# Optimization experiments

Measured on AMD Instinct MI355X. Metric: run time of the kernel, lower is better.

Reference implementation:

```python
import jax, jax.numpy as jnp
import numpy as np

H = 128  # GRU hidden dim

def gru_sequence(x_emb, W_ih, W_hh, b_ih, b_hh):
    """Run a GRU over x_emb (S, B, E); return final-step output (B, H).
    Matches torch.nn.GRU gate math:
      r = sig(W_ir x + b_ir + W_hr h + b_hr)
      z = sig(W_iz x + b_iz + W_hz h + b_hz)
      n = tanh(W_in x + b_in + r * (W_hn h + b_hn))
      h' = (1 - z) * n + z * h
    """
    S, B, E = x_emb.shape
    # Precompute input projections for all timesteps: (S, B, 3H)
    gx_all = jnp.einsum('sbe,ge->sbg', x_emb, W_ih) + b_ih

    def step(h, gx):
        gh = h @ W_hh.T + b_hh               # (B, 3H)
        r = jax.nn.sigmoid(gx[:, :H] + gh[:, :H])
        z = jax.nn.sigmoid(gx[:, H:2*H] + gh[:, H:2*H])
        n = jnp.tanh(gx[:, 2*H:] + r * gh[:, 2*H:])
        h_new = (1.0 - z) * n + z * h
        return h_new, None

    h0 = jnp.zeros((B, H), dtype=x_emb.dtype)
    h_final, _ = jax.lax.scan(step, h0, gx_all)
    return h_final  # (B, H) == out at last timestep


def setup_inputs() -> dict:
    key = jax.random.key(0)
    ks = jax.random.split(key, 12)
    S, B, V, E = 512, 512, 50000, 50
    x1 = jax.random.randint(ks[0], (S, B), 0, V, dtype=jnp.int32)
    x2 = jax.random.randint(ks[1], (S, B), 0, V, dtype=jnp.int32)
    emb = jax.random.uniform(ks[2], (V, E), jnp.float32, -0.01, 0.01)
    s = 1.0 / np.sqrt(H)
    W_ih = jax.random.uniform(ks[3], (3*H, E), jnp.float32, -s, s)
    W_hh = jax.random.uniform(ks[4], (3*H, H), jnp.float32, -s, s)
    b_ih = jax.random.uniform(ks[5], (3*H,), jnp.float32, -s, s)
    b_hh = jax.random.uniform(ks[6], (3*H,), jnp.float32, -s, s)
    s1 = 1.0 / np.sqrt(2*H)
    W1 = jax.random.uniform(ks[7], (H, 2*H), jnp.float32, -s1, s1)
    b1 = jax.random.uniform(ks[8], (H,), jnp.float32, -s1, s1)
    s2 = 1.0 / np.sqrt(H)
    W2 = jax.random.uniform(ks[9], (1, H), jnp.float32, -s2, s2)
    b2 = jax.random.uniform(ks[10], (1,), jnp.float32, -s2, s2)
    return {"x1": x1, "x2": x2, "emb": emb, "W_ih": W_ih, "W_hh": W_hh,
            "b_ih": b_ih, "b_hh": b_hh, "W1": W1, "b1": b1, "W2": W2, "b2": b2}


def reference(x1, x2, emb, W_ih, W_hh, b_ih, b_hh, W1, b1, W2, b2):
    e1 = emb[x1]  # (S, B, E)
    e2 = emb[x2]
    h1 = gru_sequence(e1, W_ih, W_hh, b_ih, b_hh)  # (B, H)
    h2 = gru_sequence(e2, W_ih, W_hh, b_ih, b_hh)  # (B, H)
    fc_in = jnp.concatenate([h1, h2], axis=-1)     # (B, 2H)
    hid = jax.nn.relu(fc_in @ W1.T + b1)
    out = jax.nn.sigmoid(hid @ W2.T + b2)          # (B, 1)
    return out
```

## Files before the change

### kernel.cpp

```cpp
#include <hip/hip_runtime.h>
#include <hip/hip_bf16.h>
#include <stdint.h>

#define S_LEN 512
#define BATCH 512
#define HID   128
#define G3    384
#define EMB   50
#define VOC   50000

#define NL2E  (-1.4426950408889634f)
#define N2L2E (-2.8853900817779268f)

typedef __attribute__((ext_vector_type(8))) short short8;
typedef __attribute__((ext_vector_type(4))) float float4v;

__device__ inline unsigned short f2bf(float f) {
  union { float f; uint32_t u; } v; v.f = f;
  uint32_t u = v.u;
  u += 0x7fffu + ((u >> 16) & 1u);
  return (unsigned short)(u >> 16);
}
__device__ inline float bf2f(unsigned short h) {
  union { uint32_t u; float f; } v; v.u = ((uint32_t)h) << 16;
  return v.f;
}
__device__ inline uint32_t fbits(float f) {
  union { float f; uint32_t u; } v; v.f = f; return v.u;
}
__device__ inline float fast_sig(float x) {
  return __builtin_amdgcn_rcpf(1.f + __expf(-x));
}

__global__ __launch_bounds__(128) void prep_wih(
    const float* __restrict__ W_ih, const float* __restrict__ b_ih,
    const float* __restrict__ b_hh, unsigned short* __restrict__ wbf,
    float* __restrict__ sbias) {
  const int nt = blockIdx.x;
  const int kf = threadIdx.x >> 6;
  const int L  = threadIdx.x & 63;
  const int q = L >> 4, ln = L & 15;
  const int g = nt * 16 + ln;
  const float sc = (g < 256) ? NL2E : N2L2E;
  const int k0 = kf * 32 + q * 8;
  short8 v;
#pragma unroll
  for (int i = 0; i < 8; ++i) {
    const int k = k0 + i;
    v[i] = (k < EMB) ? (short)f2bf(W_ih[(size_t)g * EMB + k] * sc) : (short)0;
  }
  *(short8*)(wbf + (size_t)((nt * 2 + kf) * 64 + L) * 8) = v;
  if (threadIdx.x < 16) {
    const int gg = nt * 16 + threadIdx.x;
    const float s2 = (gg < 256) ? NL2E : N2L2E;
    sbias[gg] = s2 * (b_ih[gg] + (gg < 256 ? b_hh[gg] : 0.f));
  }
}

__global__ __launch_bounds__(256) void build_gxv(
    const float* __restrict__ emb, const unsigned short* __restrict__ wbf,
    const float* __restrict__ sbias, unsigned short* __restrict__ gxv) {
  __shared__ __align__(16) unsigned short cmat[64][392];
  const int w  = threadIdx.x >> 6;
  const int L  = threadIdx.x & 63;
  const int q  = L >> 4;
  const int ln = L & 15;
  const int vbase = blockIdx.x * 64 + w * 16;
  const int vloc  = w * 16;

  const int vr = min(vbase + ln, VOC - 1);
  const float* arow = emb + (size_t)vr * EMB;
  float fa[16];
#pragma unroll
  for (int i = 0; i < 16; ++i) {
    const int k = ((i < 8) ? q * 8 : 32 + q * 8 - 8) + i;
    fa[i] = 0.f;
  }
  short8 afr0, afr1;
  {
    float f[8];
#pragma unroll
    for (int i = 0; i < 8; ++i) { const int k = q * 8 + i; f[i] = (k < EMB) ? arow[k] : 0.f; }
#pragma unroll
    for (int i = 0; i < 8; ++i) afr0[i] = (short)f2bf(f[i]);
#pragma unroll
    for (int i = 0; i < 8; ++i) { const int k = 32 + q * 8 + i; f[i] = (k < EMB) ? arow[k] : 0.f; }
#pragma unroll
    for (int i = 0; i < 8; ++i) afr1[i] = (short)f2bf(f[i]);
  }

  for (int nt = 0; nt < 24; ++nt) {
    const short8 b0 = *(const short8*)(wbf + (size_t)((nt * 2 + 0) * 64 + L) * 8);
    const short8 b1 = *(const short8*)(wbf + (size_t)((nt * 2 + 1) * 64 + L) * 8);
    const int gg = nt * 16 + ln;
    const float bias = sbias[gg];
    float4v acc = {bias, bias, bias, bias};
    acc = __builtin_amdgcn_mfma_f32_16x16x32_bf16(afr0, b0, acc, 0, 0, 0);
    acc = __builtin_amdgcn_mfma_f32_16x16x32_bf16(afr1, b1, acc, 0, 0, 0);
#pragma unroll
    for (int r = 0; r < 4; ++r)
      cmat[vloc + q * 4 + r][gg] = f2bf(acc[r]);
  }
  __syncthreads();

  for (int idx = threadIdx.x; idx < 3072; idx += 256) {
    const int row = idx / 48, c8 = idx - row * 48;
    const int vrow = blockIdx.x * 64 + row;
    if (vrow < VOC) {
      short8 v = *(const short8*)(&cmat[row][c8 * 8]);
      *(short8*)(gxv + (size_t)vrow * G3 + c8 * 8) = v;
    }
  }
}

__global__ __launch_bounds__(512) void gru_kernel(
    const int* __restrict__ x1, const int* __restrict__ x2,
    const unsigned short* __restrict__ gxv, const float* __restrict__ W_hh,
    const float* __restrict__ b_hh, float* __restrict__ fcin) {
  const int bid   = blockIdx.x;
  const int gru   = bid >> 7;
  const int chunk = bid & 127;
  const int* xs   = gru ? x2 : x1;

  const int tid = threadIdx.x;
  const int w  = tid >> 6;
  const int L  = tid & 63;
  const int q  = L >> 4;
  const int ln = L & 15;
  const int jb = w * 16;
  const int g3 = ln >> 2;
  const int n  = ln & 3;
  const int j  = jb + q * 4 + g3;
  const int ng = chunk * 4 + n;

  __shared__ __align__(16) unsigned short hbuf[2][512];

  short8 afrag[3][4];
#pragma unroll
  for (int t = 0; t < 3; ++t) {
    const float sc = (t < 2) ? NL2E : N2L2E;
    const float* wr = W_hh + (size_t)(t * 128 + jb + ln) * HID;
#pragma unroll
    for (int kf = 0; kf < 4; ++kf) {
      const int k0 = kf * 32 + q * 8;
      float4v f0 = *(const float4v*)(wr + k0);
      float4v f1 = *(const float4v*)(wr + k0 + 4);
      short8 a;
#pragma unroll
      for (int i = 0; i < 4; ++i) a[i] = (short)f2bf(f0[i] * sc);
#pragma unroll
      for (int i = 0; i < 4; ++i) a[i + 4] = (short)f2bf(f1[i] * sc);
      afrag[t][kf] = a;
    }
  }

  float4v bhn4;
#pragma unroll
  for (int r = 0; r < 4; ++r) bhn4[r] = N2L2E * b_hh[2 * 128 + jb + q * 4 + r];

  for (int idx = tid; idx < 1024; idx += 512) ((unsigned short*)hbuf)[idx] = 0;

  float h = 0.f;

  unsigned short gxr, gxz, gxnn, nr, nz, nn2;
  {
    const unsigned short* gp = gxv + (size_t)xs[ng] * G3;
    gxr = gp[j]; gxz = gp[128 + j]; gxnn = gp[256 + j];
    const unsigned short* gq = gxv + (size_t)xs[BATCH + ng] * G3;
    nr = gq[j]; nz = gq[128 + j]; nn2 = gq[256 + j];
  }
  int tokf = xs[2 * BATCH + ng];

  const int wofs = (((j >> 3) * 4 + n) << 3) + (j & 7);
  const int rofs = ((q * 4 + n) << 3);

  const bool selA = (ln & 4) != 0;
  const bool selB = (ln & 8) != 0;

  __syncthreads();

  for (int s = 0; s < S_LEN; ++s) {
    unsigned short fr, fz, fn;
    {
      const unsigned short* gp = gxv + (size_t)tokf * G3;
      fr = gp[j]; fz = gp[128 + j]; fn = gp[256 + j];
    }
    const int s3 = (s + 3 < S_LEN) ? (s + 3) : 0;
    const int tok3 = xs[s3 * BATCH + ng];

    const unsigned short* rb = hbuf[s & 1];
    short8 bfrag[4];
#pragma unroll
    for (int kf = 0; kf < 4; ++kf)
      bfrag[kf] = *(const short8*)(rb + kf * 128 + rofs);

    float vsel[3];
#pragma unroll
    for (int t = 0; t < 3; ++t) {
      float4v a0 = (t == 2) ? bhn4 : (float4v){0.f, 0.f, 0.f, 0.f};
      float4v a1 = {0.f, 0.f, 0.f, 0.f};
      a0 = __builtin_amdgcn_mfma_f32_16x16x32_bf16(afrag[t][0], bfrag[0], a0, 0, 0, 0);
      a1 = __builtin_amdgcn_mfma_f32_16x16x32_bf16(afrag[t][1], bfrag[1], a1, 0, 0, 0);
      a0 = __builtin_amdgcn_mfma_f32_16x16x32_bf16(afrag[t][2], bfrag[2], a0, 0, 0, 0);
      a1 = __builtin_amdgcn_mfma_f32_16x16x32_bf16(afrag[t][3], bfrag[3], a1, 0, 0, 0);
      const float4v acc = a0 + a1;
      const float x0 = selA ? acc[1] : acc[0];
      const float x1 = selA ? acc[3] : acc[2];
      vsel[t] = selB ? x1 : x0;
    }

    const float gr = bf2f(gxr) + vsel[0];
    const float gz = bf2f(gxz) + vsel[1];
    const float rg = __builtin_amdgcn_rcpf(1.f + __builtin_amdgcn_exp2f(gr));
    const float zg = __builtin_amdgcn_rcpf(1.f + __builtin_amdgcn_exp2f(gz));
    const float pre = bf2f(gxnn) + rg * vsel[2];
    const float sg  = __builtin_amdgcn_rcpf(1.f + __builtin_amdgcn_exp2f(pre));
    const float nn  = 2.f * sg - 1.f;
    h = zg * (h - nn) + nn;

    hbuf[(s + 1) & 1][wofs] = (unsigned short)((fbits(h) + 0x8000u) >> 16);

    asm volatile("s_waitcnt lgkmcnt(0)\n\ts_barrier" ::: "memory");

    gxr = nr; gxz = nz; gxnn = nn2;
    nr = fr; nz = fz; nn2 = fn;
    tokf = tok3;
  }

  fcin[(size_t)ng * 256 + gru * 128 + j] = h;
}

__global__ __launch_bounds__(128) void head_kernel(
    const float* __restrict__ fcin, const float* __restrict__ W1,
    const float* __restrict__ b1, const float* __restrict__ W2,
    const float* __restrict__ b2, float* __restrict__ out) {
  __shared__ float fc[256];
  __shared__ float part[2];
  const int b = blockIdx.x, t = threadIdx.x;
  fc[t]       = fcin[(size_t)b * 256 + t];
  fc[t + 128] = fcin[(size_t)b * 256 + t + 128];
  __syncthreads();

  float acc = b1[t];
#pragma unroll 8
  for (int k = 0; k < 256; ++k) acc += W1[t * 256 + k] * fc[k];
  const float hid = fmaxf(acc, 0.f);

  float v = hid * W2[t];
#pragma unroll
  for (int o = 32; o > 0; o >>= 1) v += __shfl_xor(v, o, 64);
  if ((t & 63) == 0) part[t >> 6] = v;
  __syncthreads();
  if (t == 0) {
    const float s = part[0] + part[1] + b2[0];
    out[b] = fast_sig(s);
  }
}

extern "C" void kernel_launch(void* const* d_in, const int* in_sizes, int n_in,
                              void* d_out, int out_size, void* d_ws, size_t ws_size,
                              hipStream_t stream) {
  const int*   x1   = (const int*)d_in[0];
  const int*   x2   = (const int*)d_in[1];
  const float* emb  = (const float*)d_in[2];
  const float* W_ih = (const float*)d_in[3];
  const float* W_hh = (const float*)d_in[4];
  const float* b_ih = (const float*)d_in[5];
  const float* b_hh = (const float*)d_in[6];
  const float* W1   = (const float*)d_in[7];
  const float* b1   = (const float*)d_in[8];
  const float* W2   = (const float*)d_in[9];
  const float* b2   = (const float*)d_in[10];
  float* out = (float*)d_out;

  char* ws = (char*)d_ws;
  unsigned short* gxv = (unsigned short*)ws;
  float* fcin = (float*)(ws + (size_t)VOC * G3 * 2);
  unsigned short* wbf = (unsigned short*)(ws + (size_t)VOC * G3 * 2 + 524288);
  float* sbias = (float*)(ws + (size_t)VOC * G3 * 2 + 524288 + 49152);

  prep_wih<<<24, 128, 0, stream>>>(W_ih, b_ih, b_hh, wbf, sbias);
  build_gxv<<<(VOC + 63) / 64, 256, 0, stream>>>(emb, wbf, sbias, gxv);
  gru_kernel<<<256, 512, 0, stream>>>(x1, x2, gxv, W_hh, b_hh, fcin);
  head_kernel<<<512, 128, 0, stream>>>(fcin, W1, b1, W2, b2, out);
}
```

Measured before the change: 346.7 us.

## Interleave r/z gate projections into packed 32-bit table to cut per-step gathers

```diff
diff --git a/kernel.cpp b/kernel.cpp
--- a/kernel.cpp
+++ b/kernel.cpp
@@ -21,9 +21,8 @@
   u += 0x7fffu + ((u >> 16) & 1u);
   return (unsigned short)(u >> 16);
 }
-__device__ inline float bf2f(unsigned short h) {
-  union { uint32_t u; float f; } v; v.u = ((uint32_t)h) << 16;
-  return v.f;
+__device__ inline float bitsf(uint32_t u) {
+  union { uint32_t u; float f; } v; v.u = u; return v.f;
 }
 __device__ inline uint32_t fbits(float f) {
   union { float f; uint32_t u; } v; v.f = f; return v.u;
@@ -59,8 +58,10 @@
 
 __global__ __launch_bounds__(256) void build_gxv(
     const float* __restrict__ emb, const unsigned short* __restrict__ wbf,
-    const float* __restrict__ sbias, unsigned short* __restrict__ gxv) {
-  __shared__ __align__(16) unsigned short cmat[64][392];
+    const float* __restrict__ sbias, uint32_t* __restrict__ gxrz,
+    unsigned short* __restrict__ gxn) {
+  __shared__ __align__(16) unsigned short crz[64][264];
+  __shared__ __align__(16) unsigned short cn[64][136];
   const int w  = threadIdx.x >> 6;
   const int L  = threadIdx.x & 63;
   const int q  = L >> 4;
@@ -70,25 +71,22 @@
 
   const int vr = min(vbase + ln, VOC - 1);
   const float* arow = emb + (size_t)vr * EMB;
-  float fa[16];
-#pragma unroll
-  for (int i = 0; i < 16; ++i) {
-    const int k = ((i < 8) ? q * 8 : 32 + q * 8 - 8) + i;
-    fa[i] = 0.f;
-  }
   short8 afr0, afr1;
   {
-    float f[8];
-#pragma unroll
-    for (int i = 0; i < 8; ++i) { const int k = q * 8 + i; f[i] = (k < EMB) ? arow[k] : 0.f; }
-#pragma unroll
-    for (int i = 0; i < 8; ++i) afr0[i] = (short)f2bf(f[i]);
-#pragma unroll
-    for (int i = 0; i < 8; ++i) { const int k = 32 + q * 8 + i; f[i] = (k < EMB) ? arow[k] : 0.f; }
-#pragma unroll
-    for (int i = 0; i < 8; ++i) afr1[i] = (short)f2bf(f[i]);
-  }
-
+    float f;
+#pragma unroll
+    for (int i = 0; i < 8; ++i) {
+      const int k = q * 8 + i; f = (k < EMB) ? arow[k] : 0.f;
+      afr0[i] = (short)f2bf(f);
+    }
+#pragma unroll
+    for (int i = 0; i < 8; ++i) {
+      const int k = 32 + q * 8 + i; f = (k < EMB) ? arow[k] : 0.f;
+      afr1[i] = (short)f2bf(f);
+    }
+  }
+
+#pragma unroll 2
   for (int nt = 0; nt < 24; ++nt) {
     const short8 b0 = *(const short8*)(wbf + (size_t)((nt * 2 + 0) * 64 + L) * 8);
     const short8 b1 = *(const short8*)(wbf + (size_t)((nt * 2 + 1) * 64 + L) * 8);
@@ -97,26 +95,45 @@
     float4v acc = {bias, bias, bias, bias};
     acc = __builtin_amdgcn_mfma_f32_16x16x32_bf16(afr0, b0, acc, 0, 0, 0);
     acc = __builtin_amdgcn_mfma_f32_16x16x32_bf16(afr1, b1, acc, 0, 0, 0);
-#pragma unroll
-    for (int r = 0; r < 4; ++r)
-      cmat[vloc + q * 4 + r][gg] = f2bf(acc[r]);
+    if (nt < 8) {
+      const int j = gg;
+#pragma unroll
+      for (int r = 0; r < 4; ++r) crz[vloc + q * 4 + r][2 * j] = f2bf(acc[r]);
+    } else if (nt < 16) {
+      const int j = gg - 128;
+#pragma unroll
+      for (int r = 0; r < 4; ++r) crz[vloc + q * 4 + r][2 * j + 1] = f2bf(acc[r]);
+    } else {
+      const int j = gg - 256;
+#pragma unroll
+      for (int r = 0; r < 4; ++r) cn[vloc + q * 4 + r][j] = f2bf(acc[r]);
+    }
   }
   __syncthreads();
 
-  for (int idx = threadIdx.x; idx < 3072; idx += 256) {
-    const int row = idx / 48, c8 = idx - row * 48;
+  for (int idx = threadIdx.x; idx < 2048; idx += 256) {
+    const int row = idx >> 5, c8 = idx & 31;
     const int vrow = blockIdx.x * 64 + row;
     if (vrow < VOC) {
-      short8 v = *(const short8*)(&cmat[row][c8 * 8]);
-      *(short8*)(gxv + (size_t)vrow * G3 + c8 * 8) = v;
+      short8 v = *(const short8*)(&crz[row][c8 * 8]);
+      *(short8*)((unsigned short*)gxrz + (size_t)vrow * 256 + c8 * 8) = v;
+    }
+  }
+  for (int idx = threadIdx.x; idx < 1024; idx += 256) {
+    const int row = idx >> 4, c8 = idx & 15;
+    const int vrow = blockIdx.x * 64 + row;
+    if (vrow < VOC) {
+      short8 v = *(const short8*)(&cn[row][c8 * 8]);
+      *(short8*)(gxn + (size_t)vrow * 128 + c8 * 8) = v;
     }
   }
 }
 
 __global__ __launch_bounds__(512) void gru_kernel(
     const int* __restrict__ x1, const int* __restrict__ x2,
-    const unsigned short* __restrict__ gxv, const float* __restrict__ W_hh,
-    const float* __restrict__ b_hh, float* __restrict__ fcin) {
+    const uint32_t* __restrict__ gxrz, const unsigned short* __restrict__ gxn,
+    const float* __restrict__ W_hh, const float* __restrict__ b_hh,
+    float* __restrict__ fcin) {
   const int bid   = blockIdx.x;
   const int gru   = bid >> 7;
   const int chunk = bid & 127;
@@ -162,12 +179,13 @@
 
   float h = 0.f;
 
-  unsigned short gxr, gxz, gxnn, nr, nz, nn2;
+  uint32_t rzc, rz1;
+  unsigned short nc, n1;
   {
-    const unsigned short* gp = gxv + (size_t)xs[ng] * G3;
-    gxr = gp[j]; gxz = gp[128 + j]; gxnn = gp[256 + j];
-    const unsigned short* gq = gxv + (size_t)xs[BATCH + ng] * G3;
-    nr = gq[j]; nz = gq[128 + j]; nn2 = gq[256 + j];
+    const size_t i0 = (size_t)xs[ng] * 128 + j;
+    rzc = gxrz[i0]; nc = gxn[i0];
+    const size_t i1 = (size_t)xs[BATCH + ng] * 128 + j;
+    rz1 = gxrz[i1]; n1 = gxn[i1];
   }
   int tokf = xs[2 * BATCH + ng];
 
@@ -179,12 +197,11 @@
 
   __syncthreads();
 
+#pragma unroll 2
   for (int s = 0; s < S_LEN; ++s) {
-    unsigned short fr, fz, fn;
-    {
-      const unsigned short* gp = gxv + (size_t)tokf * G3;
-      fr = gp[j]; fz = gp[128 + j]; fn = gp[256 + j];
-    }
+    const size_t i2 = (size_t)tokf * 128 + j;
+    const uint32_t rzf = gxrz[i2];
+    const unsigned short nf = gxn[i2];
     const int s3 = (s + 3 < S_LEN) ? (s + 3) : 0;
     const int tok3 = xs[s3 * BATCH + ng];
 
@@ -203,17 +220,18 @@
       a1 = __builtin_amdgcn_mfma_f32_16x16x32_bf16(afrag[t][1], bfrag[1], a1, 0, 0, 0);
       a0 = __builtin_amdgcn_mfma_f32_16x16x32_bf16(afrag[t][2], bfrag[2], a0, 0, 0, 0);
       a1 = __builtin_amdgcn_mfma_f32_16x16x32_bf16(afrag[t][3], bfrag[3], a1, 0, 0, 0);
-      const float4v acc = a0 + a1;
-      const float x0 = selA ? acc[1] : acc[0];
-      const float x1 = selA ? acc[3] : acc[2];
-      vsel[t] = selB ? x1 : x0;
-    }
-
-    const float gr = bf2f(gxr) + vsel[0];
-    const float gz = bf2f(gxz) + vsel[1];
+      const float s0 = selA ? a0[1] : a0[0];
+      const float s1 = selA ? a0[3] : a0[2];
+      const float u0 = selA ? a1[1] : a1[0];
+      const float u1 = selA ? a1[3] : a1[2];
+      vsel[t] = (selB ? s1 : s0) + (selB ? u1 : u0);
+    }
+
+    const float gr = bitsf(rzc << 16) + vsel[0];
+    const float gz = bitsf(rzc & 0xffff0000u) + vsel[1];
     const float rg = __builtin_amdgcn_rcpf(1.f + __builtin_amdgcn_exp2f(gr));
     const float zg = __builtin_amdgcn_rcpf(1.f + __builtin_amdgcn_exp2f(gz));
-    const float pre = bf2f(gxnn) + rg * vsel[2];
+    const float pre = bitsf(((uint32_t)nc) << 16) + rg * vsel[2];
     const float sg  = __builtin_amdgcn_rcpf(1.f + __builtin_amdgcn_exp2f(pre));
     const float nn  = 2.f * sg - 1.f;
     h = zg * (h - nn) + nn;
@@ -222,8 +240,8 @@
 
     asm volatile("s_waitcnt lgkmcnt(0)\n\ts_barrier" ::: "memory");
 
-    gxr = nr; gxz = nz; gxnn = nn2;
-    nr = fr; nz = fz; nn2 = fn;
+    rzc = rz1; nc = n1;
+    rz1 = rzf; n1 = nf;
     tokf = tok3;
   }
 
@@ -274,13 +292,14 @@
   float* out = (float*)d_out;
 
   char* ws = (char*)d_ws;
-  unsigned short* gxv = (unsigned short*)ws;
-  float* fcin = (float*)(ws + (size_t)VOC * G3 * 2);
-  unsigned short* wbf = (unsigned short*)(ws + (size_t)VOC * G3 * 2 + 524288);
-  float* sbias = (float*)(ws + (size_t)VOC * G3 * 2 + 524288 + 49152);
+  uint32_t*       gxrz = (uint32_t*)ws;
+  unsigned short* gxn  = (unsigned short*)(ws + 25600000);
+  float*          fcin = (float*)(ws + 38400000);
+  unsigned short* wbf  = (unsigned short*)(ws + 38924288);
+  float*          sbias= (float*)(ws + 38973440);
 
   prep_wih<<<24, 128, 0, stream>>>(W_ih, b_ih, b_hh, wbf, sbias);
-  build_gxv<<<(VOC + 63) / 64, 256, 0, stream>>>(emb, wbf, sbias, gxv);
-  gru_kernel<<<256, 512, 0, stream>>>(x1, x2, gxv, W_hh, b_hh, fcin);
+  build_gxv<<<(VOC + 63) / 64, 256, 0, stream>>>(emb, wbf, sbias, gxrz, gxn);
+  gru_kernel<<<256, 512, 0, stream>>>(x1, x2, gxrz, gxn, W_hh, b_hh, fcin);
   head_kernel<<<512, 128, 0, stream>>>(fcin, W1, b1, W2, b2, out);
 }
```

After: 411.6 us. +18.7%, slower.

## Halve GRU block to 4 waves, each computing two hidden-unit tiles

Applied to the files above, without the earlier changes.

```diff
diff --git a/kernel.cpp b/kernel.cpp
--- a/kernel.cpp
+++ b/kernel.cpp
@@ -70,23 +70,19 @@
 
   const int vr = min(vbase + ln, VOC - 1);
   const float* arow = emb + (size_t)vr * EMB;
-  float fa[16];
-#pragma unroll
-  for (int i = 0; i < 16; ++i) {
-    const int k = ((i < 8) ? q * 8 : 32 + q * 8 - 8) + i;
-    fa[i] = 0.f;
-  }
   short8 afr0, afr1;
   {
-    float f[8];
-#pragma unroll
-    for (int i = 0; i < 8; ++i) { const int k = q * 8 + i; f[i] = (k < EMB) ? arow[k] : 0.f; }
-#pragma unroll
-    for (int i = 0; i < 8; ++i) afr0[i] = (short)f2bf(f[i]);
-#pragma unroll
-    for (int i = 0; i < 8; ++i) { const int k = 32 + q * 8 + i; f[i] = (k < EMB) ? arow[k] : 0.f; }
-#pragma unroll
-    for (int i = 0; i < 8; ++i) afr1[i] = (short)f2bf(f[i]);
+    float f;
+#pragma unroll
+    for (int i = 0; i < 8; ++i) {
+      const int k = q * 8 + i; f = (k < EMB) ? arow[k] : 0.f;
+      afr0[i] = (short)f2bf(f);
+    }
+#pragma unroll
+    for (int i = 0; i < 8; ++i) {
+      const int k = 32 + q * 8 + i; f = (k < EMB) ? arow[k] : 0.f;
+      afr1[i] = (short)f2bf(f);
+    }
   }
 
   for (int nt = 0; nt < 24; ++nt) {
@@ -113,7 +109,7 @@
   }
 }
 
-__global__ __launch_bounds__(512) void gru_kernel(
+__global__ __launch_bounds__(256, 1) void gru_kernel(
     const int* __restrict__ x1, const int* __restrict__ x2,
     const unsigned short* __restrict__ gxv, const float* __restrict__ W_hh,
     const float* __restrict__ b_hh, float* __restrict__ fcin) {
@@ -127,51 +123,59 @@
   const int L  = tid & 63;
   const int q  = L >> 4;
   const int ln = L & 15;
-  const int jb = w * 16;
+  const int jb = w * 32;
   const int g3 = ln >> 2;
   const int n  = ln & 3;
-  const int j  = jb + q * 4 + g3;
+  const int j0 = jb + q * 4 + g3;
   const int ng = chunk * 4 + n;
 
   __shared__ __align__(16) unsigned short hbuf[2][512];
 
-  short8 afrag[3][4];
+  short8 afrag[3][2][4];
 #pragma unroll
   for (int t = 0; t < 3; ++t) {
     const float sc = (t < 2) ? NL2E : N2L2E;
-    const float* wr = W_hh + (size_t)(t * 128 + jb + ln) * HID;
-#pragma unroll
-    for (int kf = 0; kf < 4; ++kf) {
-      const int k0 = kf * 32 + q * 8;
-      float4v f0 = *(const float4v*)(wr + k0);
-      float4v f1 = *(const float4v*)(wr + k0 + 4);
-      short8 a;
-#pragma unroll
-      for (int i = 0; i < 4; ++i) a[i] = (short)f2bf(f0[i] * sc);
-#pragma unroll
-      for (int i = 0; i < 4; ++i) a[i + 4] = (short)f2bf(f1[i] * sc);
-      afrag[t][kf] = a;
-    }
-  }
-
-  float4v bhn4;
-#pragma unroll
-  for (int r = 0; r < 4; ++r) bhn4[r] = N2L2E * b_hh[2 * 128 + jb + q * 4 + r];
-
-  for (int idx = tid; idx < 1024; idx += 512) ((unsigned short*)hbuf)[idx] = 0;
-
-  float h = 0.f;
-
-  unsigned short gxr, gxz, gxnn, nr, nz, nn2;
+#pragma unroll
+    for (int mt = 0; mt < 2; ++mt) {
+      const float* wr = W_hh + (size_t)(t * 128 + jb + mt * 16 + ln) * HID;
+#pragma unroll
+      for (int kf = 0; kf < 4; ++kf) {
+        const int k0 = kf * 32 + q * 8;
+        float4v f0 = *(const float4v*)(wr + k0);
+        float4v f1 = *(const float4v*)(wr + k0 + 4);
+        short8 a;
+#pragma unroll
+        for (int i = 0; i < 4; ++i) a[i] = (short)f2bf(f0[i] * sc);
+#pragma unroll
+        for (int i = 0; i < 4; ++i) a[i + 4] = (short)f2bf(f1[i] * sc);
+        afrag[t][mt][kf] = a;
+      }
+    }
+  }
+
+  float4v bhn4[2];
+#pragma unroll
+  for (int mt = 0; mt < 2; ++mt)
+#pragma unroll
+    for (int r = 0; r < 4; ++r)
+      bhn4[mt][r] = N2L2E * b_hh[2 * 128 + jb + mt * 16 + q * 4 + r];
+
+  for (int idx = tid; idx < 1024; idx += 256) ((unsigned short*)hbuf)[idx] = 0;
+
+  float h0 = 0.f, h1 = 0.f;
+
+  unsigned short cr0, cr1, cz0, cz1, cn0, cn1;
+  unsigned short mr0, mr1, mz0, mz1, mn0, mn1;
   {
-    const unsigned short* gp = gxv + (size_t)xs[ng] * G3;
-    gxr = gp[j]; gxz = gp[128 + j]; gxnn = gp[256 + j];
-    const unsigned short* gq = gxv + (size_t)xs[BATCH + ng] * G3;
-    nr = gq[j]; nz = gq[128 + j]; nn2 = gq[256 + j];
+    const unsigned short* gp = gxv + (size_t)xs[ng] * G3 + j0;
+    cr0 = gp[0]; cr1 = gp[16]; cz0 = gp[128]; cz1 = gp[144]; cn0 = gp[256]; cn1 = gp[272];
+    const unsigned short* gq = gxv + (size_t)xs[BATCH + ng] * G3 + j0;
+    mr0 = gq[0]; mr1 = gq[16]; mz0 = gq[128]; mz1 = gq[144]; mn0 = gq[256]; mn1 = gq[272];
   }
   int tokf = xs[2 * BATCH + ng];
 
-  const int wofs = (((j >> 3) * 4 + n) << 3) + (j & 7);
+  const int wofs0 = (((j0 >> 3) * 4 + n) << 3) + (j0 & 7);
+  const int wofs1 = wofs0 + 64;
   const int rofs = ((q * 4 + n) << 3);
 
   const bool selA = (ln & 4) != 0;
@@ -180,10 +184,11 @@
   __syncthreads();
 
   for (int s = 0; s < S_LEN; ++s) {
-    unsigned short fr, fz, fn;
+    unsigned short fr0, fr1, fz0, fz1, fn0, fn1;
     {
-      const unsigned short* gp = gxv + (size_t)tokf * G3;
-      fr = gp[j]; fz = gp[128 + j]; fn = gp[256 + j];
+      const unsigned short* gp = gxv + (size_t)tokf * G3 + j0;
+      fr0 = gp[0]; fr1 = gp[16]; fz0 = gp[128]; fz1 = gp[144];
+      fn0 = gp[256]; fn1 = gp[272];
     }
     const int s3 = (s + 3 < S_LEN) ? (s + 3) : 0;
     const int tok3 = xs[s3 * BATCH + ng];
@@ -194,40 +199,56 @@
     for (int kf = 0; kf < 4; ++kf)
       bfrag[kf] = *(const short8*)(rb + kf * 128 + rofs);
 
-    float vsel[3];
+    float vsel[3][2];
 #pragma unroll
     for (int t = 0; t < 3; ++t) {
-      float4v a0 = (t == 2) ? bhn4 : (float4v){0.f, 0.f, 0.f, 0.f};
-      float4v a1 = {0.f, 0.f, 0.f, 0.f};
-      a0 = __builtin_amdgcn_mfma_f32_16x16x32_bf16(afrag[t][0], bfrag[0], a0, 0, 0, 0);
-      a1 = __builtin_amdgcn_mfma_f32_16x16x32_bf16(afrag[t][1], bfrag[1], a1, 0, 0, 0);
-      a0 = __builtin_amdgcn_mfma_f32_16x16x32_bf16(afrag[t][2], bfrag[2], a0, 0, 0, 0);
-      a1 = __builtin_amdgcn_mfma_f32_16x16x32_bf16(afrag[t][3], bfrag[3], a1, 0, 0, 0);
-      const float4v acc = a0 + a1;
-      const float x0 = selA ? acc[1] : acc[0];
-      const float x1 = selA ? acc[3] : acc[2];
-      vsel[t] = selB ? x1 : x0;
-    }
-
-    const float gr = bf2f(gxr) + vsel[0];
-    const float gz = bf2f(gxz) + vsel[1];
-    const float rg = __builtin_amdgcn_rcpf(1.f + __builtin_amdgcn_exp2f(gr));
-    const float zg = __builtin_amdgcn_rcpf(1.f + __builtin_amdgcn_exp2f(gz));
-    const float pre = bf2f(gxnn) + rg * vsel[2];
-    const float sg  = __builtin_amdgcn_rcpf(1.f + __builtin_amdgcn_exp2f(pre));
-    const float nn  = 2.f * sg - 1.f;
-    h = zg * (h - nn) + nn;
-
-    hbuf[(s + 1) & 1][wofs] = (unsigned short)((fbits(h) + 0x8000u) >> 16);
+#pragma unroll
+      for (int mt = 0; mt < 2; ++mt) {
+        float4v a = (t == 2) ? bhn4[mt] : (float4v){0.f, 0.f, 0.f, 0.f};
+        a = __builtin_amdgcn_mfma_f32_16x16x32_bf16(afrag[t][mt][0], bfrag[0], a, 0, 0, 0);
+        a = __builtin_amdgcn_mfma_f32_16x16x32_bf16(afrag[t][mt][1], bfrag[1], a, 0, 0, 0);
+        a = __builtin_amdgcn_mfma_f32_16x16x32_bf16(afrag[t][mt][2], bfrag[2], a, 0, 0, 0);
+        a = __builtin_amdgcn_mfma_f32_16x16x32_bf16(afrag[t][mt][3], bfrag[3], a, 0, 0, 0);
+        const float x0 = selA ? a[1] : a[0];
+        const float x1 = selA ? a[3] : a[2];
+        vsel[t][mt] = selB ? x1 : x0;
+      }
+    }
+
+    {
+      const float gr = bf2f(cr0) + vsel[0][0];
+      const float gz = bf2f(cz0) + vsel[1][0];
+      const float rg = __builtin_amdgcn_rcpf(1.f + __builtin_amdgcn_exp2f(gr));
+      const float zg = __builtin_amdgcn_rcpf(1.f + __builtin_amdgcn_exp2f(gz));
+      const float pre = bf2f(cn0) + rg * vsel[2][0];
+      const float sg  = __builtin_amdgcn_rcpf(1.f + __builtin_amdgcn_exp2f(pre));
+      const float nn  = 2.f * sg - 1.f;
+      h0 = zg * (h0 - nn) + nn;
+    }
+    {
+      const float gr = bf2f(cr1) + vsel[0][1];
+      const float gz = bf2f(cz1) + vsel[1][1];
+      const float rg = __builtin_amdgcn_rcpf(1.f + __builtin_amdgcn_exp2f(gr));
+      const float zg = __builtin_amdgcn_rcpf(1.f + __builtin_amdgcn_exp2f(gz));
+      const float pre = bf2f(cn1) + rg * vsel[2][1];
+      const float sg  = __builtin_amdgcn_rcpf(1.f + __builtin_amdgcn_exp2f(pre));
+      const float nn  = 2.f * sg - 1.f;
+      h1 = zg * (h1 - nn) + nn;
+    }
+
+    unsigned short* wbuf = hbuf[(s + 1) & 1];
+    wbuf[wofs0] = (unsigned short)((fbits(h0) + 0x8000u) >> 16);
+    wbuf[wofs1] = (unsigned short)((fbits(h1) + 0x8000u) >> 16);
 
     asm volatile("s_waitcnt lgkmcnt(0)\n\ts_barrier" ::: "memory");
 
-    gxr = nr; gxz = nz; gxnn = nn2;
-    nr = fr; nz = fz; nn2 = fn;
+    cr0 = mr0; cr1 = mr1; cz0 = mz0; cz1 = mz1; cn0 = mn0; cn1 = mn1;
+    mr0 = fr0; mr1 = fr1; mz0 = fz0; mz1 = fz1; mn0 = fn0; mn1 = fn1;
     tokf = tok3;
   }
 
-  fcin[(size_t)ng * 256 + gru * 128 + j] = h;
+  fcin[(size_t)ng * 256 + gru * 128 + j0]      = h0;
+  fcin[(size_t)ng * 256 + gru * 128 + j0 + 16] = h1;
 }
 
 __global__ __launch_bounds__(128) void head_kernel(
@@ -274,13 +295,13 @@
   float* out = (float*)d_out;
 
   char* ws = (char*)d_ws;
-  unsigned short* gxv = (unsigned short*)ws;
-  float* fcin = (float*)(ws + (size_t)VOC * G3 * 2);
-  unsigned short* wbf = (unsigned short*)(ws + (size_t)VOC * G3 * 2 + 524288);
-  float* sbias = (float*)(ws + (size_t)VOC * G3 * 2 + 524288 + 49152);
+  unsigned short* gxv  = (unsigned short*)ws;
+  float*          fcin = (float*)(ws + (size_t)VOC * G3 * 2);
+  unsigned short* wbf  = (unsigned short*)(ws + (size_t)VOC * G3 * 2 + 524288);
+  float*          sbias= (float*)(ws + (size_t)VOC * G3 * 2 + 524288 + 49152);
 
   prep_wih<<<24, 128, 0, stream>>>(W_ih, b_ih, b_hh, wbf, sbias);
   build_gxv<<<(VOC + 63) / 64, 256, 0, stream>>>(emb, wbf, sbias, gxv);
-  gru_kernel<<<256, 512, 0, stream>>>(x1, x2, gxv, W_hh, b_hh, fcin);
+  gru_kernel<<<256, 256, 0, stream>>>(x1, x2, gxv, W_hh, b_hh, fcin);
   head_kernel<<<512, 128, 0, stream>>>(fcin, W1, b1, W2, b2, out);
 }
```

New measurement: 419.3 us. 20.9% more time.
